# Kernel optimization log

Hardware: AMD Instinct MI355X
Metric: run time of the kernel (lower is better)

Reference implementation:

```python
import jax, jax.numpy as jnp
import numpy as np

NEG_INF = -1000000.0
G = 8            # window size (hardcoded: assert 8*8 == N)
DIM = 28         # hardcoded channel dim
NH = 4           # num_heads
HD = DIM // NH   # head dim = 7
PDIM = (DIM // 4) // 4  # DynamicPosBias pos_dim = (28//4)//4 = 1


def layernorm(x, g, b, eps=1e-5):
    m = jnp.mean(x, axis=-1, keepdims=True)
    v = jnp.mean((x - m) ** 2, axis=-1, keepdims=True)
    return (x - m) * jax.lax.rsqrt(v + eps) * g + b


def setup_inputs() -> dict:
    key = jax.random.key(0)
    ks = jax.random.split(key, 16)
    s = 0.05
    inp = {
        "x": jax.random.normal(ks[0], (8, 250, 250, DIM), jnp.float32),
        "qkv_w": jax.random.normal(ks[1], (3 * DIM, DIM), jnp.float32) * s,
        "qkv_b": jnp.zeros((3 * DIM,), jnp.float32),
        "proj_w": jax.random.normal(ks[2], (DIM, DIM), jnp.float32) * s,
        "proj_b": jnp.zeros((DIM,), jnp.float32),
        "pos_proj_w": jax.random.normal(ks[3], (PDIM, 2), jnp.float32) * s,
        "pos_proj_b": jnp.zeros((PDIM,), jnp.float32),
        "ln1_g": jnp.ones((PDIM,), jnp.float32),
        "ln1_b": jnp.zeros((PDIM,), jnp.float32),
        "fc1_w": jax.random.normal(ks[4], (PDIM, PDIM), jnp.float32) * s,
        "fc1_b": jnp.zeros((PDIM,), jnp.float32),
        "ln2_g": jnp.ones((PDIM,), jnp.float32),
        "ln2_b": jnp.zeros((PDIM,), jnp.float32),
        "fc2_w": jax.random.normal(ks[5], (PDIM, PDIM), jnp.float32) * s,
        "fc2_b": jnp.zeros((PDIM,), jnp.float32),
        "ln3_g": jnp.ones((PDIM,), jnp.float32),
        "ln3_b": jnp.zeros((PDIM,), jnp.float32),
        "fc3_w": jax.random.normal(ks[6], (NH, PDIM), jnp.float32) * s,
        "fc3_b": jnp.zeros((NH,), jnp.float32),
    }
    return inp


def _rel_pos_index():
    # static relative position index table, (G*G, G*G) int32 in [0, (2G-1)^2)
    coords = np.stack(np.meshgrid(np.arange(G), np.arange(G), indexing="ij"))  # (2,G,G)
    cf = coords.reshape(2, -1)                                                  # (2,GG)
    rel = cf[:, :, None] - cf[:, None, :]                                       # (2,GG,GG)
    rel = rel.transpose(1, 2, 0)
    rel[:, :, 0] += G - 1
    rel[:, :, 1] += G - 1
    rel[:, :, 0] *= 2 * G - 1
    return jnp.asarray(rel.sum(-1), jnp.int32)


def _biases():
    # (2G-1)^2 candidate relative offsets, float (225, 2)
    ph = np.arange(1 - G, G)
    b = np.stack(np.meshgrid(ph, ph, indexing="ij")).reshape(2, -1).T
    return jnp.asarray(b, jnp.float32)


def reference(x, qkv_w, qkv_b, proj_w, proj_b,
              pos_proj_w, pos_proj_b,
              ln1_g, ln1_b, fc1_w, fc1_b,
              ln2_g, ln2_b, fc2_w, fc2_b,
              ln3_g, ln3_b, fc3_w, fc3_b):
    B, H, W, C = x.shape
    pad_b = (-H) % G
    pad_r = (-W) % G
    x = jnp.pad(x, ((0, 0), (0, pad_b), (0, pad_r), (0, 0)))
    Hd, Wd = H + pad_b, W + pad_r
    nH, nW = Hd // G, Wd // G
    nP = nH * nW
    GG = G * G

    # window partition -> (B*nP, GG, C)
    xw = x.reshape(B, nH, G, nW, G, C).transpose(0, 1, 3, 2, 4, 5).reshape(B * nP, GG, C)

    # padding mask over keys, per window: (nP, 1, GG) additive
    m2d = jnp.zeros((Hd, Wd), jnp.float32)
    if pad_b > 0:
        m2d = m2d.at[-pad_b:, :].set(-1.0)
    if pad_r > 0:
        m2d = m2d.at[:, -pad_r:].set(-1.0)
    mw = m2d.reshape(nH, G, nW, G).transpose(0, 2, 1, 3).reshape(nP, GG)
    attn_mask = jnp.where(mw[:, None, :] < 0, NEG_INF, 0.0)  # (nP,1,GG)

    # qkv projection
    qkv = xw @ qkv_w.T + qkv_b                    # (B_, GG, 3C)
    qkv = qkv.reshape(B * nP, GG, 3, NH, HD).transpose(2, 0, 3, 1, 4)
    q, k, v = qkv[0], qkv[1], qkv[2]              # (B_, NH, GG, HD)
    scale = HD ** (-0.5)
    attn = jnp.einsum("bhnd,bhmd->bhnm", q * scale, k)  # (B_, NH, GG, GG)

    # dynamic relative position bias: tiny MLP over (2G-1)^2 offsets
    t = _biases() @ pos_proj_w.T + pos_proj_b                      # (225, PDIM)
    t = layernorm(t, ln1_g, ln1_b)
    t = jax.nn.relu(t) @ fc1_w.T + fc1_b
    t = layernorm(t, ln2_g, ln2_b)
    t = jax.nn.relu(t) @ fc2_w.T + fc2_b
    t = layernorm(t, ln3_g, ln3_b)
    pos = jax.nn.relu(t) @ fc3_w.T + fc3_b                         # (225, NH)
    rpb = pos[_rel_pos_index()]                                    # (GG, GG, NH)
    rpb = rpb.transpose(2, 0, 1)                                   # (NH, GG, GG)
    attn = attn + rpb[None]

    # add padding mask then softmax
    attn = attn.reshape(B, nP, NH, GG, GG) + attn_mask[None, :, None, :, :]
    attn = jax.nn.softmax(attn.reshape(B * nP, NH, GG, GG), axis=-1)

    out = jnp.einsum("bhnm,bhmd->bnhd", attn, v).reshape(B * nP, GG, C)
    out = out @ proj_w.T + proj_b

    # un-window, crop padding, flatten spatial
    out = out.reshape(B, nH, nW, G, G, C).transpose(0, 1, 3, 2, 4, 5).reshape(B, Hd, Wd, C)
    out = out[:, :H, :W, :].reshape(B, H * W, C)
    return out
```

## Files before the change

### kernel.cpp

```cpp
#include <hip/hip_runtime.h>

#define HW 250

typedef float    f32x16 __attribute__((ext_vector_type(16)));
typedef _Float16 f16x8  __attribute__((ext_vector_type(8)));
typedef unsigned u32x4  __attribute__((ext_vector_type(4)));

__device__ inline unsigned pkrtz(float a, float b) {
    return __builtin_bit_cast(unsigned, __builtin_amdgcn_cvt_pkrtz(a, b));
}
__device__ inline f16x8 as_f16x8(u32x4 v) { return __builtin_bit_cast(f16x8, v); }

__global__ __launch_bounds__(256, 4)
void win_attn(const float* __restrict__ x,
              const float* __restrict__ qkv_w,
              const float* __restrict__ qkv_b,
              const float* __restrict__ proj_w,
              const float* __restrict__ proj_b,
              float* __restrict__ out)
{
    __shared__ __align__(16) short s_x16[64 * 40];
    __shared__ __align__(16) short s_wa[128 * 40];
    __shared__ __align__(16) float s_pw[28 * 28];
    __shared__ __align__(16) short s_vt[4 * 512];
    __shared__ __align__(16) float s_oT[28 * 66];
    __shared__ float s_pb[28];

    const int t    = threadIdx.x;
    const int lane = t & 63;
    const int w    = t >> 6;
    const int s_   = lane >> 5;
    const int col  = lane & 31;
    const int blk = blockIdx.x;
    const int b   = blk >> 10;
    const int p   = blk & 1023;
    const int r0  = (p >> 5) << 3;
    const int c0  = (p & 31) << 3;

    for (int i = t; i < 196; i += 256)
        *(float4*)&s_pw[i * 4] = *(const float4*)&proj_w[i * 4];
    if (t < 28) s_pb[t] = proj_b[t];

    #pragma unroll
    for (int it = 0; it < 2; ++it) {
        const int i = t + it * 256;
        const int n = i >> 3, g = i & 7;
        if (g < 7) {
            const int r = r0 + (n >> 3), c = c0 + (n & 7);
            float4 v = make_float4(0.f, 0.f, 0.f, 0.f);
            if (r < HW && c < HW)
                v = *(const float4*)&x[((b * HW + r) * HW + c) * 28 + g * 4];
            uint2 h; h.x = pkrtz(v.x, v.y); h.y = pkrtz(v.z, v.w);
            *(uint2*)&s_x16[n * 40 + g * 4] = h;
        } else {
            uint2 h; h.x = 0x00003C00u; h.y = 0u;
            *(uint2*)&s_x16[n * 40 + 28] = h;
        }
    }

    {
        const int rowid = t >> 1, half = t & 1;
        const int slab = rowid >> 5, a = rowid & 31;
        int src = -1; float sc = 1.f;
        if (a < 7)               { src = slab * 7 + a;              sc = 0.5452538663326288f; }
        else if (a >= 8 && a < 15)  { src = 28 + slab * 7 + (a - 8);  }
        else if (a >= 16 && a < 23) { src = 56 + slab * 7 + (a - 16); }
        u32x4 o0 = {0u,0u,0u,0u}, o1 = {0u,0u,0u,0u};
        if (src >= 0) {
            const float* wr = &qkv_w[src * 28];
            if (half == 0) {
                const float4 A = *(const float4*)&wr[0],  B = *(const float4*)&wr[4];
                const float4 C = *(const float4*)&wr[8],  D = *(const float4*)&wr[12];
                o0.x = pkrtz(A.x*sc, A.y*sc); o0.y = pkrtz(A.z*sc, A.w*sc);
                o0.z = pkrtz(B.x*sc, B.y*sc); o0.w = pkrtz(B.z*sc, B.w*sc);
                o1.x = pkrtz(C.x*sc, C.y*sc); o1.y = pkrtz(C.z*sc, C.w*sc);
                o1.z = pkrtz(D.x*sc, D.y*sc); o1.w = pkrtz(D.z*sc, D.w*sc);
            } else {
                const float4 A = *(const float4*)&wr[16], B = *(const float4*)&wr[20];
                const float4 C = *(const float4*)&wr[24];
                const float bias = qkv_b[src];
                o0.x = pkrtz(A.x*sc, A.y*sc); o0.y = pkrtz(A.z*sc, A.w*sc);
                o0.z = pkrtz(B.x*sc, B.y*sc); o0.w = pkrtz(B.z*sc, B.w*sc);
                o1.x = pkrtz(C.x*sc, C.y*sc); o1.y = pkrtz(C.z*sc, C.w*sc);
                o1.z = pkrtz(bias*sc, 0.f);   o1.w = 0u;
            }
        }
        *(u32x4*)&s_wa[rowid * 40 + half * 16 + 0] = o0;
        *(u32x4*)&s_wa[rowid * 40 + half * 16 + 8] = o1;
    }
    __syncthreads();

    u32x4 qf0, qf1, kf0, kf1;
    {
        const f16x8 wfa = *(const f16x8*)&s_wa[(w * 32 + col) * 40 + s_ * 8];
        const f16x8 wfb = *(const f16x8*)&s_wa[(w * 32 + col) * 40 + 16 + s_ * 8];
        #pragma unroll
        for (int tile = 0; tile < 2; ++tile) {
            const int tok = tile * 32 + col;
            const f16x8 xb0 = *(const f16x8*)&s_x16[tok * 40 + s_ * 8];
            const f16x8 xb1 = *(const f16x8*)&s_x16[tok * 40 + 16 + s_ * 8];
            f32x16 C;
            #pragma unroll
            for (int r = 0; r < 16; ++r) C[r] = 0.f;
            C = __builtin_amdgcn_mfma_f32_32x32x16_f16(wfa, xb0, C, 0, 0, 0);
            C = __builtin_amdgcn_mfma_f32_32x32x16_f16(wfb, xb1, C, 0, 0, 0);
            const unsigned qA = pkrtz(C[0], C[1]);
            const unsigned qB = pkrtz(C[2], s_ ? 0.f : C[3]);
            const unsigned kA = pkrtz(C[4], C[5]);
            const unsigned kB = pkrtz(C[6], s_ ? 0.f : C[7]);
            const unsigned qAx = (unsigned)__shfl_xor((int)qA, 32);
            const unsigned qBx = (unsigned)__shfl_xor((int)qB, 32);
            const unsigned kAx = (unsigned)__shfl_xor((int)kA, 32);
            const unsigned kBx = (unsigned)__shfl_xor((int)kB, 32);
            u32x4 qf, kf;
            qf.x = s_ ? 0u : qA;  qf.y = s_ ? 0u : qB;
            qf.z = s_ ? 0u : qAx; qf.w = s_ ? 0u : qBx;
            kf.x = s_ ? 0u : kA;  kf.y = s_ ? 0u : kB;
            kf.z = s_ ? 0u : kAx; kf.w = s_ ? 0u : kBx;
            #pragma unroll
            for (int j = 0; j < 4; ++j) {
                const int d = 4 * s_ + j;
                if (d < 7) {
                    const unsigned hv = pkrtz(C[8 + j], 0.f);
                    s_vt[w * 512 + ((d * 64 + tok) ^ (d << 3))] = (short)(hv & 0xffff);
                }
            }
            if (tile == 0) { qf0 = qf; kf0 = kf; } else { qf1 = qf; kf1 = kf; }
        }
    }
    __syncthreads();

    {
        const int vr = min(8, HW - r0), vc = min(8, HW - c0);
        const bool edge = (vr < 8) || (vc < 8);
        const int dd = (col < 7) ? col : 6;
        const f16x8 kfa = as_f16x8(kf0), kfb = as_f16x8(kf1);

        #pragma unroll
        for (int qt = 0; qt < 2; ++qt) {
            const f16x8 qfrag = as_f16x8(qt == 0 ? qf0 : qf1);
            f32x16 a0, a1;
            #pragma unroll
            for (int r = 0; r < 16; ++r) { a0[r] = 0.f; a1[r] = 0.f; }
            a0 = __builtin_amdgcn_mfma_f32_32x32x16_f16(kfa, qfrag, a0, 0, 0, 0);
            a1 = __builtin_amdgcn_mfma_f32_32x32x16_f16(kfb, qfrag, a1, 0, 0, 0);
            if (edge) {
                #pragma unroll
                for (int r = 0; r < 16; ++r) {
                    const int kc  = (r & 3) + 4 * s_;
                    const int kr0 = (r >> 2), kr1 = 4 + (r >> 2);
                    a0[r] = (kr0 < vr && kc < vc) ? a0[r] : -1e30f;
                    a1[r] = (kr1 < vr && kc < vc) ? a1[r] : -1e30f;
                }
            }
            float m = -1e30f;
            #pragma unroll
            for (int r = 0; r < 16; ++r) { m = fmaxf(m, a0[r]); m = fmaxf(m, a1[r]); }
            m = fmaxf(m, __shfl_xor(m, 32));
            float sum = 0.f;
            #pragma unroll
            for (int r = 0; r < 16; ++r) {
                a0[r] = __builtin_amdgcn_exp2f(a0[r] - m); sum += a0[r];
                a1[r] = __builtin_amdgcn_exp2f(a1[r] - m); sum += a1[r];
            }
            sum += __shfl_xor(sum, 32);
            const float inv = __builtin_amdgcn_rcpf(sum);

            f32x16 O;
            #pragma unroll
            for (int r = 0; r < 16; ++r) O[r] = 0.f;
            #pragma unroll
            for (int tt = 0; tt < 4; ++tt) {
                const f16x8 vfrag = *(const f16x8*)&s_vt[w * 512 + ((dd * 64 + 16 * tt + 8 * s_) ^ (dd << 3))];
                const int bb = 8 * (tt & 1);
                float p0,p1,p2,p3,p4,p5,p6,p7;
                if (tt < 2) { p0=a0[bb+0];p1=a0[bb+1];p2=a0[bb+2];p3=a0[bb+3];
                              p4=a0[bb+4];p5=a0[bb+5];p6=a0[bb+6];p7=a0[bb+7]; }
                else        { p0=a1[bb+0];p1=a1[bb+1];p2=a1[bb+2];p3=a1[bb+3];
                              p4=a1[bb+4];p5=a1[bb+5];p6=a1[bb+6];p7=a1[bb+7]; }
                const unsigned X0 = pkrtz(p0, p1), X1 = pkrtz(p2, p3);
                const unsigned Y0 = pkrtz(p4, p5), Y1 = pkrtz(p6, p7);
                const unsigned sX0 = (unsigned)__shfl_xor((int)X0, 32);
                const unsigned sX1 = (unsigned)__shfl_xor((int)X1, 32);
                const unsigned sY0 = (unsigned)__shfl_xor((int)Y0, 32);
                const unsigned sY1 = (unsigned)__shfl_xor((int)Y1, 32);
                u32x4 pf;
                pf.x = s_ ? sY0 : X0;
                pf.y = s_ ? sY1 : X1;
                pf.z = s_ ? Y0  : sX0;
                pf.w = s_ ? Y1  : sX1;
                O = __builtin_amdgcn_mfma_f32_32x32x16_f16(vfrag, as_f16x8(pf), O, 0, 0, 0);
            }
            #pragma unroll
            for (int r = 0; r < 4; ++r) {
                const int d = r + 4 * s_;
                if (d < 7) s_oT[(w * 7 + d) * 66 + 32 * qt + col] = O[r] * inv;
            }
        }
    }
    __syncthreads();

    {
        const int n = t >> 2, q4 = t & 3;
        const int r = r0 + (n >> 3), c = c0 + (n & 7);
        if (r < HW && c < HW) {
            float xr[28];
            #pragma unroll
            for (int cc = 0; cc < 28; ++cc) xr[cc] = s_oT[cc * 66 + n];
            float* dst = &out[((b * HW + r) * HW + c) * 28 + q4 * 7];
            #pragma unroll
            for (int j = 0; j < 7; ++j) {
                const int co = q4 * 7 + j;
                const float* wr = &s_pw[co * 28];
                float acc = s_pb[co];
                #pragma unroll
                for (int g = 0; g < 7; ++g) {
                    const float4 ww = *(const float4*)&wr[g * 4];
                    acc += xr[g*4+0]*ww.x + xr[g*4+1]*ww.y + xr[g*4+2]*ww.z + xr[g*4+3]*ww.w;
                }
                dst[j] = acc;
            }
        }
    }
}

extern "C" void kernel_launch(void* const* d_in, const int* in_sizes, int n_in,
                              void* d_out, int out_size, void* d_ws, size_t ws_size,
                              hipStream_t stream) {
    const float* x      = (const float*)d_in[0];
    const float* qkv_w  = (const float*)d_in[1];
    const float* qkv_b  = (const float*)d_in[2];
    const float* proj_w = (const float*)d_in[3];
    const float* proj_b = (const float*)d_in[4];
    float* out = (float*)d_out;

    dim3 grid(8 * 32 * 32);
    dim3 block(256);
    hipLaunchKernelGGL(win_attn, grid, block, 0, stream,
                       x, qkv_w, qkv_b, proj_w, proj_b, out);
}
```

Measured before the change: 63.39 us.

## Run output projection on MFMA in fp16 and pool shared memory for occupancy

The scalar fp32 output projection is replaced by two f16 MFMA 32x32x16 ops per wave. The attention output and proj weights are now stored in fp16 in shared memory. All shared buffers are merged into one aliased pool, with the output buffer reusing the x region, to cut LDS per block, and launch bounds are raised from 4 to 7 blocks per CU. This removes many FMA instructions and shrinks LDS, in exchange for extra fp16 rounding in the projection and possible register pressure at the higher occupancy target.

```diff
diff --git a/kernel.cpp b/kernel.cpp
--- a/kernel.cpp
+++ b/kernel.cpp
@@ -11,7 +11,12 @@
 }
 __device__ inline f16x8 as_f16x8(u32x4 v) { return __builtin_bit_cast(f16x8, v); }
 
-__global__ __launch_bounds__(256, 4)
+#define OFF_X   0
+#define OFF_WA  2560
+#define OFF_PW  7680
+#define OFF_VT  8960
+
+__global__ __launch_bounds__(256, 7)
 void win_attn(const float* __restrict__ x,
               const float* __restrict__ qkv_w,
               const float* __restrict__ qkv_b,
@@ -19,12 +24,13 @@
               const float* __restrict__ proj_b,
               float* __restrict__ out)
 {
-    __shared__ __align__(16) short s_x16[64 * 40];
-    __shared__ __align__(16) short s_wa[128 * 40];
-    __shared__ __align__(16) float s_pw[28 * 28];
-    __shared__ __align__(16) short s_vt[4 * 512];
-    __shared__ __align__(16) float s_oT[28 * 66];
-    __shared__ float s_pb[28];
+    __shared__ __align__(16) short s_pool[11008];
+    __shared__ __align__(16) float s_pb[28];
+    short* const s_x16  = s_pool + OFF_X;
+    short* const s_wa   = s_pool + OFF_WA;
+    short* const s_pw16 = s_pool + OFF_PW;
+    short* const s_vt   = s_pool + OFF_VT;
+    short* const s_o16  = s_pool + OFF_X;
 
     const int t    = threadIdx.x;
     const int lane = t & 63;
@@ -37,8 +43,19 @@
     const int r0  = (p >> 5) << 3;
     const int c0  = (p & 31) << 3;
 
-    for (int i = t; i < 196; i += 256)
-        *(float4*)&s_pw[i * 4] = *(const float4*)&proj_w[i * 4];
+    {
+        const int co = t >> 3, g = t & 7;
+        uint2 h; h.x = 0u; h.y = 0u;
+        if (g < 7) {
+            if (co < 28) {
+                const float4 v = *(const float4*)&proj_w[co * 28 + g * 4];
+                h.x = pkrtz(v.x, v.y); h.y = pkrtz(v.z, v.w);
+            }
+            *(uint2*)&s_pw16[co * 40 + g * 4] = h;
+        } else {
+            *(uint2*)&s_pw16[co * 40 + 28] = h;
+        }
+    }
     if (t < 28) s_pb[t] = proj_b[t];
 
     #pragma unroll
@@ -194,31 +211,41 @@
             #pragma unroll
             for (int r = 0; r < 4; ++r) {
                 const int d = r + 4 * s_;
-                if (d < 7) s_oT[(w * 7 + d) * 66 + 32 * qt + col] = O[r] * inv;
+                if (d < 7) {
+                    const unsigned hv = pkrtz(O[r] * inv, 0.f);
+                    s_o16[(32 * qt + col) * 40 + w * 7 + d] = (short)(hv & 0xffff);
+                }
             }
         }
     }
     __syncthreads();
 
     {
-        const int n = t >> 2, q4 = t & 3;
-        const int r = r0 + (n >> 3), c = c0 + (n & 7);
-        if (r < HW && c < HW) {
-            float xr[28];
-            #pragma unroll
-            for (int cc = 0; cc < 28; ++cc) xr[cc] = s_oT[cc * 66 + n];
-            float* dst = &out[((b * HW + r) * HW + c) * 28 + q4 * 7];
-            #pragma unroll
-            for (int j = 0; j < 7; ++j) {
-                const int co = q4 * 7 + j;
-                const float* wr = &s_pw[co * 28];
-                float acc = s_pb[co];
-                #pragma unroll
-                for (int g = 0; g < 7; ++g) {
-                    const float4 ww = *(const float4*)&wr[g * 4];
-                    acc += xr[g*4+0]*ww.x + xr[g*4+1]*ww.y + xr[g*4+2]*ww.z + xr[g*4+3]*ww.w;
-                }
-                dst[j] = acc;
+        const int tile = w & 1, ch = w >> 1;
+        const int tok  = tile * 32 + col;
+        const f16x8 ob0 = *(const f16x8*)&s_o16[tok * 40 + 8 * s_];
+        const f16x8 ob1 = *(const f16x8*)&s_o16[tok * 40 + 16 + 8 * s_];
+        const f16x8 wa0 = *(const f16x8*)&s_pw16[col * 40 + 8 * s_];
+        const f16x8 wa1 = *(const f16x8*)&s_pw16[col * 40 + 16 + 8 * s_];
+        f32x16 C;
+        #pragma unroll
+        for (int r = 0; r < 16; ++r) C[r] = 0.f;
+        C = __builtin_amdgcn_mfma_f32_32x32x16_f16(wa0, ob0, C, 0, 0, 0);
+        C = __builtin_amdgcn_mfma_f32_32x32x16_f16(wa1, ob1, C, 0, 0, 0);
+        const int rr = r0 + (tok >> 3), cc = c0 + (tok & 7);
+        if (rr < HW && cc < HW) {
+            float* dst = &out[((b * HW + rr) * HW + cc) * 28];
+            #pragma unroll
+            for (int j2 = 0; j2 < 2; ++j2) {
+                const int j  = 2 * ch + j2;
+                const int co = 8 * j + 4 * s_;
+                if (co < 28) {
+                    const float4 bias = *(const float4*)&s_pb[co];
+                    float4 o;
+                    o.x = C[4*j+0] + bias.x; o.y = C[4*j+1] + bias.y;
+                    o.z = C[4*j+2] + bias.z; o.w = C[4*j+3] + bias.w;
+                    *(float4*)&dst[co] = o;
+                }
             }
         }
     }
```

After: 58.26 us. 8.1% less time.
